# Performance work log

Measured on AMD Instinct MI355X. Metric: run time of the kernel, lower is better.

Reference implementation:

```python
import jax, jax.numpy as jnp
import numpy as np

B, T, H, W, C = 4, 8, 64, 64, 256
WS = (2, 8, 8)        # window size (t,h,w); T,H,W chosen divisible -> no padding path
SS = (1, 4, 4)        # shift = window//2 (use_shift=True)
NH = 8
HD = C // NH
HID = int(C * 2.0)    # mlp_ratio=2.0
N = WS[0] * WS[1] * WS[2]          # 128 tokens per window
SCALE = HD ** -0.5
RPB_SIZE = (2 * WS[0] - 1) * (2 * WS[1] - 1) * (2 * WS[2] - 1)  # 675


def _rel_index(ws):
    coords = np.stack(np.meshgrid(np.arange(ws[0]), np.arange(ws[1]), np.arange(ws[2]), indexing='ij'))
    cf = coords.reshape(3, -1)
    rc = (cf[:, :, None] - cf[:, None, :]).transpose(1, 2, 0).astype(np.int64)
    rc[..., 0] += ws[0] - 1
    rc[..., 1] += ws[1] - 1
    rc[..., 2] += ws[2] - 1
    rc[..., 0] *= (2 * ws[1] - 1) * (2 * ws[2] - 1)
    rc[..., 1] *= 2 * ws[2] - 1
    return rc.sum(-1)  # [N, N]

REL_IDX = jnp.asarray(_rel_index(WS))


def _attn_mask(t, h, w, ws, ss):
    img = np.zeros((t, h, w), np.float32)
    cnt = 0
    for ts in (slice(0, -ws[0]), slice(-ws[0], -ss[0]), slice(-ss[0], None)):
        for hs in (slice(0, -ws[1]), slice(-ws[1], -ss[1]), slice(-ss[1], None)):
            for wsl in (slice(0, -ws[2]), slice(-ws[2], -ss[2]), slice(-ss[2], None)):
                img[ts, hs, wsl] = cnt
                cnt += 1
    mw = img.reshape(t // ws[0], ws[0], h // ws[1], ws[1], w // ws[2], ws[2])
    mw = mw.transpose(0, 2, 4, 1, 3, 5).reshape(-1, ws[0] * ws[1] * ws[2])  # [nW, N]
    am = mw[:, None, :] - mw[:, :, None]
    return np.where(am != 0, -100.0, 0.0).astype(np.float32)  # [nW, N, N]

ATTN_MASK = jnp.asarray(_attn_mask(T, H, W, WS, SS))


def layernorm(x, g, b):
    m = x.mean(-1, keepdims=True)
    v = x.var(-1, keepdims=True)
    return (x - m) / jnp.sqrt(v + 1e-5) * g + b


def win_part(x):
    # [B,T,H,W,C] -> [B*nW, N, C]
    x = x.reshape(B, T // WS[0], WS[0], H // WS[1], WS[1], W // WS[2], WS[2], C)
    return x.transpose(0, 1, 3, 5, 2, 4, 6, 7).reshape(-1, N, C)


def win_rev(w):
    x = w.reshape(B, T // WS[0], H // WS[1], W // WS[2], WS[0], WS[1], WS[2], C)
    return x.transpose(0, 1, 4, 2, 5, 3, 6, 7).reshape(B, T, H, W, C)


def win_attn(xw, rpb, qkv_w, qkv_b, proj_w, proj_b, mask):
    Bw = xw.shape[0]
    qkv = (xw @ qkv_w + qkv_b).reshape(Bw, N, 3, NH, HD).transpose(2, 0, 3, 1, 4)
    q, k, v = qkv[0] * SCALE, qkv[1], qkv[2]          # [Bw, NH, N, HD]
    a = jnp.einsum('bhnd,bhmd->bhnm', q, k)
    bias = rpb[REL_IDX.reshape(-1)].reshape(N, N, NH).transpose(2, 0, 1)
    a = a + bias[None]
    if mask is not None:
        nW = mask.shape[0]
        a = (a.reshape(Bw // nW, nW, NH, N, N) + mask[None, :, None]).reshape(Bw, NH, N, N)
    a = jax.nn.softmax(a, -1)
    o = jnp.einsum('bhnm,bhmd->bhnd', a, v).transpose(0, 2, 1, 3).reshape(Bw, N, C)
    return o @ proj_w + proj_b


def mlp(x, w1, b1, w2, b2):
    return jax.nn.gelu(x @ w1 + b1, approximate=False) @ w2 + b2


def setup_inputs():
    key = jax.random.key(0)
    ks = jax.random.split(key, 16)
    s = 0.02
    inp = {
        'x': jax.random.normal(ks[0], (B, T, H, W, C), jnp.float32),
        'rpb1': jax.random.normal(ks[1], (RPB_SIZE, NH), jnp.float32) * s,
        'qkv_w1': jax.random.normal(ks[2], (C, 3 * C), jnp.float32) * s,
        'qkv_b1': jnp.zeros((3 * C,), jnp.float32),
        'proj_w1': jax.random.normal(ks[3], (C, C), jnp.float32) * s,
        'proj_b1': jnp.zeros((C,), jnp.float32),
        'rpb2': jax.random.normal(ks[4], (RPB_SIZE, NH), jnp.float32) * s,
        'qkv_w2': jax.random.normal(ks[5], (C, 3 * C), jnp.float32) * s,
        'qkv_b2': jnp.zeros((3 * C,), jnp.float32),
        'proj_w2': jax.random.normal(ks[6], (C, C), jnp.float32) * s,
        'proj_b2': jnp.zeros((C,), jnp.float32),
        'g1': jnp.ones((C,), jnp.float32), 'be1': jnp.zeros((C,), jnp.float32),
        'g2': jnp.ones((C,), jnp.float32), 'be2': jnp.zeros((C,), jnp.float32),
        'g3': jnp.ones((C,), jnp.float32), 'be3': jnp.zeros((C,), jnp.float32),
        'g4': jnp.ones((C,), jnp.float32), 'be4': jnp.zeros((C,), jnp.float32),
        'm1w1': jax.random.normal(ks[7], (C, HID), jnp.float32) * s,
        'm1b1': jnp.zeros((HID,), jnp.float32),
        'm1w2': jax.random.normal(ks[8], (HID, C), jnp.float32) * s,
        'm1b2': jnp.zeros((C,), jnp.float32),
        'm2w1': jax.random.normal(ks[9], (C, HID), jnp.float32) * s,
        'm2b1': jnp.zeros((HID,), jnp.float32),
        'm2w2': jax.random.normal(ks[10], (HID, C), jnp.float32) * s,
        'm2b2': jnp.zeros((C,), jnp.float32),
    }
    return inp


def reference(x, rpb1, qkv_w1, qkv_b1, proj_w1, proj_b1,
              rpb2, qkv_w2, qkv_b2, proj_w2, proj_b2,
              g1, be1, g2, be2, g3, be3, g4, be4,
              m1w1, m1b1, m1w2, m1b2, m2w1, m2b1, m2w2, m2b2):
    # block 1: plain window attention (no shift)
    shortcut = x
    xw = win_part(layernorm(x, g1, be1))
    aw = win_attn(xw, rpb1, qkv_w1, qkv_b1, proj_w1, proj_b1, None)
    x = shortcut + win_rev(aw)
    x = x + mlp(layernorm(x, g2, be2), m1w1, m1b1, m1w2, m1b2)
    # block 2: shifted window attention with mask
    shortcut = x
    xn = layernorm(x, g3, be3)
    sx = jnp.roll(xn, (-SS[0], -SS[1], -SS[2]), axis=(1, 2, 3))
    aw = win_attn(win_part(sx), rpb2, qkv_w2, qkv_b2, proj_w2, proj_b2, ATTN_MASK)
    x = shortcut + jnp.roll(win_rev(aw), SS, axis=(1, 2, 3))
    x = x + mlp(layernorm(x, g4, be4), m2w1, m2b1, m2w2, m2b2)
    return x
```

## Files before the change

kernel.cpp:

```cpp
#include <hip/hip_runtime.h>
#include <stdint.h>

typedef __bf16 bf16_t;
using bf16x8 = __attribute__((ext_vector_type(8))) __bf16;
using f32x4  = __attribute__((ext_vector_type(4))) float;

#define DEVINL __device__ __forceinline__

DEVINL void gload_lds16(const bf16_t* g, char* l) {
  __builtin_amdgcn_global_load_lds(
      (const __attribute__((address_space(1))) void*)g,
      (__attribute__((address_space(3))) void*)l, 16, 0, 0);
}

DEVINL uint2 pack4(float a, float b, float c, float d) {
  union { bf16_t h[4]; uint2 u; } pk;
  pk.h[0] = (bf16_t)a; pk.h[1] = (bf16_t)b;
  pk.h[2] = (bf16_t)c; pk.h[3] = (bf16_t)d;
  return pk.u;
}

__global__ void conv_w(const float* __restrict__ w, bf16_t* __restrict__ wt,
                       int kshift, int N, int total) {
  int i = blockIdx.x * 256 + threadIdx.x;
  if (i >= total) return;
  int n = i >> kshift, k = i & ((1 << kshift) - 1);
  wt[i] = (bf16_t)w[(size_t)k * N + n];
}

__global__ void build_bias1(const float* __restrict__ rpb, bf16_t* __restrict__ tab) {
  int idx = blockIdx.x * 256 + threadIdx.x;
  int n = idx >> 7, m = idx & 127;
  int it1 = n >> 6, ih1 = (n >> 3) & 7, iw1 = n & 7;
  int it2 = m >> 6, ih2 = (m >> 3) & 7, iw2 = m & 7;
  int ridx = (it1 - it2 + 1) * 225 + (ih1 - ih2 + 7) * 15 + (iw1 - iw2 + 7);
#pragma unroll
  for (int h = 0; h < 8; ++h)
    tab[(h << 14) + idx] = (bf16_t)rpb[ridx * 8 + h];
}

__global__ void build_bias2(const float* __restrict__ rpb, bf16_t* __restrict__ tab) {
  int idx = blockIdx.x * 256 + threadIdx.x;
  int cat = blockIdx.y;
  int ct = cat >> 2, ch = (cat >> 1) & 1, cw = cat & 1;
  int n = idx >> 7, m = idx & 127;
  int it1 = n >> 6, ih1 = (n >> 3) & 7, iw1 = n & 7;
  int it2 = m >> 6, ih2 = (m >> 3) & 7, iw2 = m & 7;
  int rt1 = ct ? (it1 == 0 ? 1 : 2) : 0;
  int rh1 = ch ? (ih1 < 4 ? 1 : 2) : 0;
  int rw1 = cw ? (iw1 < 4 ? 1 : 2) : 0;
  int rt2 = ct ? (it2 == 0 ? 1 : 2) : 0;
  int rh2 = ch ? (ih2 < 4 ? 1 : 2) : 0;
  int rw2 = cw ? (iw2 < 4 ? 1 : 2) : 0;
  float msk = (rt1 != rt2 || rh1 != rh2 || rw1 != rw2) ? -100.f : 0.f;
  int ridx = (it1 - it2 + 1) * 225 + (ih1 - ih2 + 7) * 15 + (iw1 - iw2 + 7);
#pragma unroll
  for (int h = 0; h < 8; ++h)
    tab[(size_t)((cat * 8 + h) << 14) + idx] = (bf16_t)(rpb[ridx * 8 + h] + msk);
}

__global__ __launch_bounds__(256)
void ln_kernel(const float* __restrict__ x, const float* __restrict__ g,
               const float* __restrict__ b, bf16_t* __restrict__ out) {
  int row = blockIdx.x * 4 + (threadIdx.x >> 6);
  int lane = threadIdx.x & 63;
  float4 v = *((const float4*)(x + (size_t)row * 256) + lane);
  float s = v.x + v.y + v.z + v.w;
#pragma unroll
  for (int m = 1; m < 64; m <<= 1) s += __shfl_xor(s, m);
  float mean = s * 0.00390625f;
  float dx = v.x - mean, dy = v.y - mean, dz = v.z - mean, dw = v.w - mean;
  float s2 = dx * dx + dy * dy + dz * dz + dw * dw;
#pragma unroll
  for (int m = 1; m < 64; m <<= 1) s2 += __shfl_xor(s2, m);
  float rstd = rsqrtf(s2 * 0.00390625f + 1e-5f);
  float4 gv = *((const float4*)g + lane);
  float4 bv = *((const float4*)b + lane);
  union { bf16_t h[4]; uint2 u; } pk;
  pk.h[0] = (bf16_t)(dx * rstd * gv.x + bv.x);
  pk.h[1] = (bf16_t)(dy * rstd * gv.y + bv.y);
  pk.h[2] = (bf16_t)(dz * rstd * gv.z + bv.z);
  pk.h[3] = (bf16_t)(dw * rstd * gv.w + bv.w);
  *(uint2*)(out + (size_t)row * 256 + lane * 4) = pk.u;
}

template <int EPI>
__global__ __launch_bounds__(256, 2)
void gemm_bt(const bf16_t* __restrict__ A, const bf16_t* __restrict__ Bt,
             const float* __restrict__ bias, const float* __restrict__ resid,
             void* __restrict__ outp, int M, int N, int K, float qscale, int qcols) {
  __shared__ __align__(16) char ldsA[16384];
  __shared__ __align__(16) char ldsB[16384];
  const int tid = threadIdx.x;
  const int lane = tid & 63, wid = tid >> 6;
  const int l15 = lane & 15, l4 = lane >> 4;
  const int tn = blockIdx.x, tm = blockIdx.y;
  const int wm = wid >> 1, wn = wid & 1;

  f32x4 acc[4][4] = {};
  const int nK = K >> 6;
  const size_t arow0 = (size_t)(tm * 128) * K;

  for (int kt = 0; kt < nK; ++kt) {
    const int kb = kt * 64;
#pragma unroll
    for (int i = 0; i < 4; ++i) {
      int c = i * 256 + tid;
      int row = c >> 3, slot = c & 7;
      int ss = slot ^ (row & 7);
      gload_lds16(A + arow0 + (size_t)row * K + kb + ss * 8,
                  ldsA + (i * 256 + wid * 64) * 16);
      gload_lds16(Bt + (size_t)(tn * 128 + row) * K + kb + ss * 8,
                  ldsB + (i * 256 + wid * 64) * 16);
    }
    __syncthreads();
    bf16x8 af[4][2], bfr[4][2];
#pragma unroll
    for (int mi = 0; mi < 4; ++mi) {
      int row = wm * 64 + mi * 16 + l15;
      int sw = (row & 7) << 4;
#pragma unroll
      for (int kk = 0; kk < 2; ++kk)
        af[mi][kk] = *(const bf16x8*)(ldsA + row * 128 + ((kk * 64 + l4 * 16) ^ sw));
    }
#pragma unroll
    for (int ni = 0; ni < 4; ++ni) {
      int row = wn * 64 + ni * 16 + l15;
      int sw = (row & 7) << 4;
#pragma unroll
      for (int kk = 0; kk < 2; ++kk)
        bfr[ni][kk] = *(const bf16x8*)(ldsB + row * 128 + ((kk * 64 + l4 * 16) ^ sw));
    }
#pragma unroll
    for (int kk = 0; kk < 2; ++kk)
#pragma unroll
      for (int mi = 0; mi < 4; ++mi)
#pragma unroll
        for (int ni = 0; ni < 4; ++ni)
          acc[mi][ni] = __builtin_amdgcn_mfma_f32_16x16x32_bf16(
              af[mi][kk], bfr[ni][kk], acc[mi][ni], 0, 0, 0);
    __syncthreads();
  }

#pragma unroll
  for (int mi = 0; mi < 4; ++mi) {
#pragma unroll
    for (int ni = 0; ni < 4; ++ni) {
      int col = tn * 128 + wn * 64 + ni * 16 + l15;
      float bv = bias[col];
#pragma unroll
      for (int v = 0; v < 4; ++v) {
        int row = tm * 128 + wm * 64 + mi * 16 + l4 * 4 + v;
        float val = acc[mi][ni][v] + bv;
        size_t idx = (size_t)row * N + col;
        if constexpr (EPI == 0) {
          if (col < qcols) val *= qscale;
          ((bf16_t*)outp)[idx] = (bf16_t)val;
        } else if constexpr (EPI == 1) {
          ((float*)outp)[idx] = resid[idx] + val;
        } else {
          ((bf16_t*)outp)[idx] =
              (bf16_t)(0.5f * val * (1.0f + erff(val * 0.7071067811865475f)));
        }
      }
    }
  }
}

DEVINL int tok3(int it, int ih, int iw, int tw, int hw, int ww, int b8, bool SH) {
  int t, h, w;
  if (SH) { t = (tw * 2 + it + 1) & 7; h = (hw * 8 + ih + 4) & 63; w = (ww * 8 + iw + 4) & 63; }
  else    { t =  tw * 2 + it;          h =  hw * 8 + ih;           w =  ww * 8 + iw; }
  return ((b8 + t) << 12) + (h << 6) + w;
}

template <bool SHIFTED>
__global__ __launch_bounds__(256, 4)
void attn_kernel(const bf16_t* __restrict__ qkv, const bf16_t* __restrict__ btab,
                 bf16_t* __restrict__ o) {
  __shared__ __align__(16) char VtL[8192];
  __shared__ __align__(16) char PL[32768];

  const int tid = threadIdx.x, lane = tid & 63, wid = tid >> 6;
  const int l15 = lane & 15, l4 = lane >> 4;
  const int blk = blockIdx.x;
  const int head = blk & 7;
  const int win = blk >> 3;
  const int b8 = (win >> 8) * 8, rem = win & 255;
  const int tw = rem >> 6, hw = (rem >> 3) & 7, ww = rem & 7;
  const int hoff = head << 5;

  const bf16_t* bt;
  if (SHIFTED) {
    int cat = ((tw == 3) ? 4 : 0) | ((hw == 7) ? 2 : 0) | ((ww == 7) ? 1 : 0);
    bt = btab + ((size_t)(cat * 8 + head) << 14);
  } else {
    bt = btab + ((size_t)head << 14);
  }

  bf16x8 kf[8], qf[2];
  int tokq[2];
#pragma unroll
  for (int ki = 0; ki < 8; ++ki) {
    int tok = tok3(ki >> 2, (ki * 2 + (l15 >> 3)) & 7, l15 & 7, tw, hw, ww, b8, SHIFTED);
    kf[ki] = *(const bf16x8*)(qkv + (size_t)tok * 768 + 256 + hoff + l4 * 8);
  }
#pragma unroll
  for (int qi = 0; qi < 2; ++qi) {
    int g = wid * 2 + qi;
    tokq[qi] = tok3(g >> 2, (g * 2 + (l15 >> 3)) & 7, l15 & 7, tw, hw, ww, b8, SHIFTED);
    qf[qi] = *(const bf16x8*)(qkv + (size_t)tokq[qi] * 768 + hoff + l4 * 8);
  }

  {
    int tv = tok3(lane >> 5, (lane >> 2) & 7, (lane & 3) * 2, tw, hw, ww, b8, SHIFTED);
    const bf16_t* vp = qkv + (size_t)tv * 768 + 512 + hoff + wid * 8;
    bf16x8 va = *(const bf16x8*)vp;
    bf16x8 vb = *(const bf16x8*)(vp + 768);
#pragma unroll
    for (int j = 0; j < 8; ++j) {
      int d = wid * 8 + j;
      union { bf16_t h[2]; uint u; } pk2;
      pk2.h[0] = va[j]; pk2.h[1] = vb[j];
      *(uint*)(VtL + d * 256 + ((lane * 4) ^ (j << 4))) = pk2.u;
    }
  }
  __syncthreads();

  f32x4 st[8][2];
#pragma unroll
  for (int ki = 0; ki < 8; ++ki)
#pragma unroll
    for (int qi = 0; qi < 2; ++qi) {
      int q = wid * 32 + qi * 16 + l15;
      uint2 bu = *(const uint2*)(bt + (q << 7) + ki * 16 + l4 * 4);
      f32x4 c;
      c[0] = __uint_as_float(bu.x << 16);
      c[1] = __uint_as_float(bu.x & 0xffff0000u);
      c[2] = __uint_as_float(bu.y << 16);
      c[3] = __uint_as_float(bu.y & 0xffff0000u);
      st[ki][qi] = __builtin_amdgcn_mfma_f32_16x16x32_bf16(kf[ki], qf[qi], c, 0, 0, 0);
    }

  char* PLw = PL + wid * 8192;
#pragma unroll
  for (int qi = 0; qi < 2; ++qi) {
    float mx = -1e30f;
#pragma unroll
    for (int ki = 0; ki < 8; ++ki)
#pragma unroll
      for (int v = 0; v < 4; ++v) mx = fmaxf(mx, st[ki][qi][v]);
    mx = fmaxf(mx, __shfl_xor(mx, 16));
    mx = fmaxf(mx, __shfl_xor(mx, 32));
    float sum = 0.f;
#pragma unroll
    for (int ki = 0; ki < 8; ++ki)
#pragma unroll
      for (int v = 0; v < 4; ++v) {
        float e = __expf(st[ki][qi][v] - mx);
        st[ki][qi][v] = e;
        sum += e;
      }
    sum += __shfl_xor(sum, 16);
    sum += __shfl_xor(sum, 32);
    float inv = 1.0f / sum;
    int r = qi * 16 + l15;
    int sw = (l15 & 7) << 5;
#pragma unroll
    for (int ki = 0; ki < 8; ++ki) {
      uint2 pk = pack4(st[ki][qi][0] * inv, st[ki][qi][1] * inv,
                       st[ki][qi][2] * inv, st[ki][qi][3] * inv);
      *(uint2*)(PLw + r * 256 + ((ki * 32 + l4 * 8) ^ sw)) = pk;
    }
  }

  f32x4 oacc[2][2] = {};
#pragma unroll
  for (int kk = 0; kk < 4; ++kk) {
    bf16x8 vf[2], pf[2];
#pragma unroll
    for (int dj = 0; dj < 2; ++dj) {
      int d = dj * 16 + l15;
      vf[dj] = *(const bf16x8*)(VtL + d * 256 + ((kk * 64 + l4 * 16) ^ ((d & 7) << 4)));
    }
#pragma unroll
    for (int qi = 0; qi < 2; ++qi) {
      int r = qi * 16 + l15;
      pf[qi] = *(const bf16x8*)(PLw + r * 256 + ((kk * 64 + l4 * 16) ^ ((l15 & 7) << 5)));
    }
#pragma unroll
    for (int dj = 0; dj < 2; ++dj)
#pragma unroll
      for (int qi = 0; qi < 2; ++qi)
        oacc[dj][qi] = __builtin_amdgcn_mfma_f32_16x16x32_bf16(vf[dj], pf[qi], oacc[dj][qi], 0, 0, 0);
  }

#pragma unroll
  for (int qi = 0; qi < 2; ++qi) {
#pragma unroll
    for (int dj = 0; dj < 2; ++dj) {
      uint2 pk = pack4(oacc[dj][qi][0], oacc[dj][qi][1],
                       oacc[dj][qi][2], oacc[dj][qi][3]);
      *(uint2*)(o + (size_t)tokq[qi] * 256 + hoff + dj * 16 + l4 * 4) = pk;
    }
  }
}

extern "C" void kernel_launch(void* const* d_in, const int* in_sizes, int n_in,
                              void* d_out, int out_size, void* d_ws, size_t ws_size,
                              hipStream_t stream) {
  const float* x       = (const float*)d_in[0];
  const float* rpb1    = (const float*)d_in[1];
  const float* qkv_w1  = (const float*)d_in[2];
  const float* qkv_b1  = (const float*)d_in[3];
  const float* proj_w1 = (const float*)d_in[4];
  const float* proj_b1 = (const float*)d_in[5];
  const float* rpb2    = (const float*)d_in[6];
  const float* qkv_w2  = (const float*)d_in[7];
  const float* qkv_b2  = (const float*)d_in[8];
  const float* proj_w2 = (const float*)d_in[9];
  const float* proj_b2 = (const float*)d_in[10];
  const float* g1  = (const float*)d_in[11];
  const float* be1 = (const float*)d_in[12];
  const float* g2  = (const float*)d_in[13];
  const float* be2 = (const float*)d_in[14];
  const float* g3  = (const float*)d_in[15];
  const float* be3 = (const float*)d_in[16];
  const float* g4  = (const float*)d_in[17];
  const float* be4 = (const float*)d_in[18];
  const float* m1w1 = (const float*)d_in[19];
  const float* m1b1 = (const float*)d_in[20];
  const float* m1w2 = (const float*)d_in[21];
  const float* m1b2 = (const float*)d_in[22];
  const float* m2w1 = (const float*)d_in[23];
  const float* m2b1 = (const float*)d_in[24];
  const float* m2w2 = (const float*)d_in[25];
  const float* m2b2 = (const float*)d_in[26];
  float* out = (float*)d_out;

  char* ws = (char*)d_ws;
  bf16_t* qkvb = (bf16_t*)ws;
  bf16_t* xn   = (bf16_t*)(ws + 201326592ull);
  bf16_t* wts  = (bf16_t*)(ws + 268435456ull);
  bf16_t* btab1 = (bf16_t*)(ws + 270532608ull);
  bf16_t* btab2 = (bf16_t*)(ws + 270794752ull);

  bf16_t* qw1t = wts;
  bf16_t* pw1t = wts + 196608;
  bf16_t* a1t  = wts + 262144;
  bf16_t* a2t  = wts + 393216;
  bf16_t* qw2t = wts + 524288;
  bf16_t* pw2t = wts + 720896;
  bf16_t* c1t  = wts + 786432;
  bf16_t* c2t  = wts + 917504;

  conv_w<<<768, 256, 0, stream>>>(qkv_w1, qw1t, 8, 768, 196608);
  conv_w<<<256, 256, 0, stream>>>(proj_w1, pw1t, 8, 256, 65536);
  conv_w<<<512, 256, 0, stream>>>(m1w1, a1t, 8, 512, 131072);
  conv_w<<<512, 256, 0, stream>>>(m1w2, a2t, 9, 256, 131072);
  conv_w<<<768, 256, 0, stream>>>(qkv_w2, qw2t, 8, 768, 196608);
  conv_w<<<256, 256, 0, stream>>>(proj_w2, pw2t, 8, 256, 65536);
  conv_w<<<512, 256, 0, stream>>>(m2w1, c1t, 8, 512, 131072);
  conv_w<<<512, 256, 0, stream>>>(m2w2, c2t, 9, 256, 131072);
  build_bias1<<<64, 256, 0, stream>>>(rpb1, btab1);
  build_bias2<<<dim3(64, 8), 256, 0, stream>>>(rpb2, btab2);

  const float SC = 0.17677669529663687f;
  const int M = 131072;

  ln_kernel<<<32768, 256, 0, stream>>>(x, g1, be1, xn);
  gemm_bt<0><<<dim3(6, 1024), 256, 0, stream>>>(xn, qw1t, qkv_b1, nullptr, qkvb, M, 768, 256, SC, 256);
  attn_kernel<false><<<8192, 256, 0, stream>>>(qkvb, btab1, xn);
  gemm_bt<1><<<dim3(2, 1024), 256, 0, stream>>>(xn, pw1t, proj_b1, x, out, M, 256, 256, 1.f, 0);
  ln_kernel<<<32768, 256, 0, stream>>>(out, g2, be2, xn);
  gemm_bt<2><<<dim3(4, 1024), 256, 0, stream>>>(xn, a1t, m1b1, nullptr, qkvb, M, 512, 256, 1.f, 0);
  gemm_bt<1><<<dim3(2, 1024), 256, 0, stream>>>(qkvb, a2t, m1b2, out, out, M, 256, 512, 1.f, 0);

  ln_kernel<<<32768, 256, 0, stream>>>(out, g3, be3, xn);
  gemm_bt<0><<<dim3(6, 1024), 256, 0, stream>>>(xn, qw2t, qkv_b2, nullptr, qkvb, M, 768, 256, SC, 256);
  attn_kernel<true><<<8192, 256, 0, stream>>>(qkvb, btab2, xn);
  gemm_bt<1><<<dim3(2, 1024), 256, 0, stream>>>(xn, pw2t, proj_b2, out, out, M, 256, 256, 1.f, 0);
  ln_kernel<<<32768, 256, 0, stream>>>(out, g4, be4, xn);
  gemm_bt<2><<<dim3(4, 1024), 256, 0, stream>>>(xn, c1t, m2b1, nullptr, qkvb, M, 512, 256, 1.f, 0);
  gemm_bt<1><<<dim3(2, 1024), 256, 0, stream>>>(qkvb, c2t, m2b2, out, out, M, 256, 512, 1.f, 0);
}
```

Before: 1.297 ms.

## Scatter QKV GEMM output into window order and gather back in proj epilogue

The QKV GEMM epilogue now writes each row to its window-partitioned (and shifted) position, so the attention kernel reads contiguous window rows instead of computing scattered token addresses. The projection GEMM maps its window-ordered A rows back to raster order when writing the residual output. This removes the per-token address arithmetic and the non-contiguous gathers in attention, and moves the permutation cost into GEMM epilogue stores, which are now row-scattered per 4-row group.

Result: no change. 1.299 ms (+0.2%).

```diff
diff --git a/kernel.cpp b/kernel.cpp
--- a/kernel.cpp
+++ b/kernel.cpp
@@ -18,6 +18,29 @@
   pk.h[0] = (bf16_t)a; pk.h[1] = (bf16_t)b;
   pk.h[2] = (bf16_t)c; pk.h[3] = (bf16_t)d;
   return pk.u;
+}
+
+DEVINL int ras2win(int r, int sh) {
+  int b = r >> 15;
+  int t = (r >> 12) & 7, h = (r >> 6) & 63, w = r & 63;
+  int pt = sh ? ((t + 7) & 7) : t;
+  int ph = sh ? ((h + 60) & 63) : h;
+  int pw = sh ? ((w + 60) & 63) : w;
+  int w8 = ((pt >> 1) << 6) | ((ph >> 3) << 3) | (pw >> 3);
+  int n  = ((pt & 1) << 6) | ((ph & 7) << 3) | (pw & 7);
+  return (b << 15) | (w8 << 7) | n;
+}
+DEVINL int win2ras(int pr, int sh) {
+  int b = pr >> 15;
+  int w8 = (pr >> 7) & 255;
+  int n = pr & 127;
+  int pt = ((w8 >> 6) << 1) | (n >> 6);
+  int ph = ((w8 >> 3) & 7) * 8 + ((n >> 3) & 7);
+  int pw = (w8 & 7) * 8 + (n & 7);
+  int t = sh ? ((pt + 1) & 7) : pt;
+  int h = sh ? ((ph + 4) & 63) : ph;
+  int w = sh ? ((pw + 4) & 63) : pw;
+  return ((b * 8 + t) << 12) | (h << 6) | w;
 }
 
 __global__ void conv_w(const float* __restrict__ w, bf16_t* __restrict__ wt,
@@ -84,7 +107,7 @@
   *(uint2*)(out + (size_t)row * 256 + lane * 4) = pk.u;
 }
 
-template <int EPI>
+template <int EPI, int PMODE>
 __global__ __launch_bounds__(256, 2)
 void gemm_bt(const bf16_t* __restrict__ A, const bf16_t* __restrict__ Bt,
              const float* __restrict__ bias, const float* __restrict__ resid,
@@ -142,17 +165,26 @@
     __syncthreads();
   }
 
+  float bvs[4];
+#pragma unroll
+  for (int ni = 0; ni < 4; ++ni)
+    bvs[ni] = bias[tn * 128 + wn * 64 + ni * 16 + l15];
+
 #pragma unroll
   for (int mi = 0; mi < 4; ++mi) {
 #pragma unroll
-    for (int ni = 0; ni < 4; ++ni) {
-      int col = tn * 128 + wn * 64 + ni * 16 + l15;
-      float bv = bias[col];
-#pragma unroll
-      for (int v = 0; v < 4; ++v) {
-        int row = tm * 128 + wm * 64 + mi * 16 + l4 * 4 + v;
-        float val = acc[mi][ni][v] + bv;
-        size_t idx = (size_t)row * N + col;
+    for (int v = 0; v < 4; ++v) {
+      int row = tm * 128 + wm * 64 + mi * 16 + l4 * 4 + v;
+      int orow = row;
+      if constexpr (PMODE != 0) {
+        if constexpr (EPI == 0) orow = ras2win(row, PMODE == 2);
+        else                    orow = win2ras(row, PMODE == 2);
+      }
+#pragma unroll
+      for (int ni = 0; ni < 4; ++ni) {
+        int col = tn * 128 + wn * 64 + ni * 16 + l15;
+        float val = acc[mi][ni][v] + bvs[ni];
+        size_t idx = (size_t)orow * N + col;
         if constexpr (EPI == 0) {
           if (col < qcols) val *= qscale;
           ((bf16_t*)outp)[idx] = (bf16_t)val;
@@ -167,13 +199,6 @@
   }
 }
 
-DEVINL int tok3(int it, int ih, int iw, int tw, int hw, int ww, int b8, bool SH) {
-  int t, h, w;
-  if (SH) { t = (tw * 2 + it + 1) & 7; h = (hw * 8 + ih + 4) & 63; w = (ww * 8 + iw + 4) & 63; }
-  else    { t =  tw * 2 + it;          h =  hw * 8 + ih;           w =  ww * 8 + iw; }
-  return ((b8 + t) << 12) + (h << 6) + w;
-}
-
 template <bool SHIFTED>
 __global__ __launch_bounds__(256, 4)
 void attn_kernel(const bf16_t* __restrict__ qkv, const bf16_t* __restrict__ btab,
@@ -186,35 +211,29 @@
   const int blk = blockIdx.x;
   const int head = blk & 7;
   const int win = blk >> 3;
-  const int b8 = (win >> 8) * 8, rem = win & 255;
-  const int tw = rem >> 6, hw = (rem >> 3) & 7, ww = rem & 7;
   const int hoff = head << 5;
+  const bf16_t* base = qkv + (size_t)(win * 128) * 768;
 
   const bf16_t* bt;
   if (SHIFTED) {
-    int cat = ((tw == 3) ? 4 : 0) | ((hw == 7) ? 2 : 0) | ((ww == 7) ? 1 : 0);
+    int w8 = win & 255;
+    int cat = (((w8 >> 6) == 3) ? 4 : 0) | ((((w8 >> 3) & 7) == 7) ? 2 : 0) |
+              (((w8 & 7) == 7) ? 1 : 0);
     bt = btab + ((size_t)(cat * 8 + head) << 14);
   } else {
     bt = btab + ((size_t)head << 14);
   }
 
   bf16x8 kf[8], qf[2];
-  int tokq[2];
-#pragma unroll
-  for (int ki = 0; ki < 8; ++ki) {
-    int tok = tok3(ki >> 2, (ki * 2 + (l15 >> 3)) & 7, l15 & 7, tw, hw, ww, b8, SHIFTED);
-    kf[ki] = *(const bf16x8*)(qkv + (size_t)tok * 768 + 256 + hoff + l4 * 8);
-  }
-#pragma unroll
-  for (int qi = 0; qi < 2; ++qi) {
-    int g = wid * 2 + qi;
-    tokq[qi] = tok3(g >> 2, (g * 2 + (l15 >> 3)) & 7, l15 & 7, tw, hw, ww, b8, SHIFTED);
-    qf[qi] = *(const bf16x8*)(qkv + (size_t)tokq[qi] * 768 + hoff + l4 * 8);
-  }
+#pragma unroll
+  for (int ki = 0; ki < 8; ++ki)
+    kf[ki] = *(const bf16x8*)(base + (size_t)(ki * 16 + l15) * 768 + 256 + hoff + l4 * 8);
+#pragma unroll
+  for (int qi = 0; qi < 2; ++qi)
+    qf[qi] = *(const bf16x8*)(base + (size_t)(wid * 32 + qi * 16 + l15) * 768 + hoff + l4 * 8);
 
   {
-    int tv = tok3(lane >> 5, (lane >> 2) & 7, (lane & 3) * 2, tw, hw, ww, b8, SHIFTED);
-    const bf16_t* vp = qkv + (size_t)tv * 768 + 512 + hoff + wid * 8;
+    const bf16_t* vp = base + (size_t)(lane * 2) * 768 + 512 + hoff + wid * 8;
     bf16x8 va = *(const bf16x8*)vp;
     bf16x8 vb = *(const bf16x8*)(vp + 768);
 #pragma unroll
@@ -297,11 +316,12 @@
 
 #pragma unroll
   for (int qi = 0; qi < 2; ++qi) {
+    size_t tau = (size_t)(win * 128 + wid * 32 + qi * 16 + l15);
 #pragma unroll
     for (int dj = 0; dj < 2; ++dj) {
       uint2 pk = pack4(oacc[dj][qi][0], oacc[dj][qi][1],
                        oacc[dj][qi][2], oacc[dj][qi][3]);
-      *(uint2*)(o + (size_t)tokq[qi] * 256 + hoff + dj * 16 + l4 * 4) = pk;
+      *(uint2*)(o + tau * 256 + hoff + dj * 16 + l4 * 4) = pk;
     }
   }
 }
@@ -369,18 +389,18 @@
   const int M = 131072;
 
   ln_kernel<<<32768, 256, 0, stream>>>(x, g1, be1, xn);
-  gemm_bt<0><<<dim3(6, 1024), 256, 0, stream>>>(xn, qw1t, qkv_b1, nullptr, qkvb, M, 768, 256, SC, 256);
+  gemm_bt<0, 1><<<dim3(6, 1024), 256, 0, stream>>>(xn, qw1t, qkv_b1, nullptr, qkvb, M, 768, 256, SC, 256);
   attn_kernel<false><<<8192, 256, 0, stream>>>(qkvb, btab1, xn);
-  gemm_bt<1><<<dim3(2, 1024), 256, 0, stream>>>(xn, pw1t, proj_b1, x, out, M, 256, 256, 1.f, 0);
+  gemm_bt<1, 1><<<dim3(2, 1024), 256, 0, stream>>>(xn, pw1t, proj_b1, x, out, M, 256, 256, 1.f, 0);
   ln_kernel<<<32768, 256, 0, stream>>>(out, g2, be2, xn);
-  gemm_bt<2><<<dim3(4, 1024), 256, 0, stream>>>(xn, a1t, m1b1, nullptr, qkvb, M, 512, 256, 1.f, 0);
-  gemm_bt<1><<<dim3(2, 1024), 256, 0, stream>>>(qkvb, a2t, m1b2, out, out, M, 256, 512, 1.f, 0);
+  gemm_bt<2, 0><<<dim3(4, 1024), 256, 0, stream>>>(xn, a1t, m1b1, nullptr, qkvb, M, 512, 256, 1.f, 0);
+  gemm_bt<1, 0><<<dim3(2, 1024), 256, 0, stream>>>(qkvb, a2t, m1b2, out, out, M, 256, 512, 1.f, 0);
 
   ln_kernel<<<32768, 256, 0, stream>>>(out, g3, be3, xn);
-  gemm_bt<0><<<dim3(6, 1024), 256, 0, stream>>>(xn, qw2t, qkv_b2, nullptr, qkvb, M, 768, 256, SC, 256);
+  gemm_bt<0, 2><<<dim3(6, 1024), 256, 0, stream>>>(xn, qw2t, qkv_b2, nullptr, qkvb, M, 768, 256, SC, 256);
   attn_kernel<true><<<8192, 256, 0, stream>>>(qkvb, btab2, xn);
-  gemm_bt<1><<<dim3(2, 1024), 256, 0, stream>>>(xn, pw2t, proj_b2, out, out, M, 256, 256, 1.f, 0);
+  gemm_bt<1, 2><<<dim3(2, 1024), 256, 0, stream>>>(xn, pw2t, proj_b2, out, out, M, 256, 256, 1.f, 0);
   ln_kernel<<<32768, 256, 0, stream>>>(out, g4, be4, xn);
-  gemm_bt<2><<<dim3(4, 1024), 256, 0, stream>>>(xn, c1t, m2b1, nullptr, qkvb, M, 512, 256, 1.f, 0);
-  gemm_bt<1><<<dim3(2, 1024), 256, 0, stream>>>(qkvb, c2t, m2b2, out, out, M, 256, 512, 1.f, 0);
-}
+  gemm_bt<2, 0><<<dim3(4, 1024), 256, 0, stream>>>(xn, c1t, m2b1, nullptr, qkvb, M, 512, 256, 1.f, 0);
+  gemm_bt<1, 0><<<dim3(2, 1024), 256, 0, stream>>>(qkvb, c2t, m2b2, out, out, M, 256, 512, 1.f, 0);
+}
```
